# Optimization experiments

Hardware: AMD Instinct MI355X
Metric: run time of the kernel (lower is better)

## Reference

```python
import jax, jax.numpy as jnp
import numpy as np

HEADS = 16
CHUNK = 128  # chunked (mathematically exact) form of the causal cumsum linear attention
EPS = 0.001


def _linear_attention(q, k, v):
    # q, k, v: (B, H, L, d); q, k already SiLU-featurized
    B, H, L, d = q.shape
    Nc = L // CHUNK
    qc = q.reshape(B, H, Nc, CHUNK, d)
    kc = k.reshape(B, H, Nc, CHUNK, d)
    vc = v.reshape(B, H, Nc, CHUNK, d)

    # inter-chunk running state: S = cumsum of k (x) v over previous chunks, z = cumsum of k
    kv_chunk = jnp.einsum('bhncd,bhnce->bhnde', kc, vc)        # (B,H,Nc,d,d)
    S = jnp.cumsum(kv_chunk, axis=2) - kv_chunk                 # exclusive cumsum
    k_sum = kc.sum(axis=3)                                      # (B,H,Nc,d)
    z = jnp.cumsum(k_sum, axis=2) - k_sum                       # exclusive cumsum

    # intra-chunk causal part
    scores = jnp.einsum('bhnid,bhnjd->bhnij', qc, kc)           # (B,H,Nc,C,C)
    mask = jnp.tril(jnp.ones((CHUNK, CHUNK), dtype=bool))
    scores = jnp.where(mask, scores, jnp.zeros((), scores.dtype))
    num = jnp.einsum('bhnij,bhnje->bhnie', scores, vc)
    num = num + jnp.einsum('bhnid,bhnde->bhnie', qc, S)

    k_cum_local = jnp.cumsum(kc, axis=3)                        # within-chunk cumsum of k
    den = jnp.einsum('bhnid,bhnid->bhni', qc, k_cum_local)
    den = den + jnp.einsum('bhnid,bhnd->bhni', qc, z)

    out = num / jnp.maximum(den, EPS)[..., None]
    return out.reshape(B, H, L, d)


def setup_inputs() -> dict:
    key = jax.random.key(0)
    ks = jax.random.split(key, 9)
    D = 1024
    B, L = 4, 2048
    s = 0.02  # init scale
    return {
        'x':  jax.random.normal(ks[0], (B, L, D), dtype=jnp.float32),
        'Wq': jax.random.normal(ks[1], (D, D), dtype=jnp.float32) * s,
        'bq': jnp.zeros((D,), dtype=jnp.float32),
        'Wk': jax.random.normal(ks[2], (D, D), dtype=jnp.float32) * s,
        'bk': jnp.zeros((D,), dtype=jnp.float32),
        'Wv': jax.random.normal(ks[3], (D, D), dtype=jnp.float32) * s,
        'bv': jnp.zeros((D,), dtype=jnp.float32),
        'Wo': jax.random.normal(ks[4], (D, D), dtype=jnp.float32) * s,
        'bo': jnp.zeros((D,), dtype=jnp.float32),
    }


def reference(x, Wq, bq, Wk, bk, Wv, bv, Wo, bo):
    B, L, D = x.shape
    H = HEADS
    d = D // H
    # torch Linear: y = x @ W.T + b
    q = jax.nn.silu(x @ Wq.T + bq).reshape(B, L, H, d).transpose(0, 2, 1, 3)
    k = jax.nn.silu(x @ Wk.T + bk).reshape(B, L, H, d).transpose(0, 2, 1, 3)
    v = (x @ Wv.T + bv).reshape(B, L, H, d).transpose(0, 2, 1, 3)
    out = _linear_attention(q, k, v)                  # (B,H,L,d)
    out = out.transpose(0, 2, 1, 3).reshape(B, L, D)
    return out @ Wo.T + bo
```

## Files before the change

kernel.cpp:

```cpp
#include <hip/hip_runtime.h>
#include <math.h>

#define D_MODEL 1024
#define HEADS   16
#define HDIM    64
#define CHUNK   128
#define B_SZ    4
#define L_SEQ   2048
#define NCHUNK  16
#define NTOK    8192
#define EPS_DEN 1e-3f

typedef _Float16 half8 __attribute__((ext_vector_type(8)));
typedef _Float16 half4 __attribute__((ext_vector_type(4)));
typedef float    f32x4 __attribute__((ext_vector_type(4)));

__device__ __forceinline__ void gld_lds16(const void* g, void* l) {
    __builtin_amdgcn_global_load_lds(
        (const __attribute__((address_space(1))) void*)g,
        (__attribute__((address_space(3))) void*)l, 16, 0, 0);
}

__global__ __launch_bounds__(256) void prep(
    const float* __restrict__ x,  const float* __restrict__ Wq,
    const float* __restrict__ Wk, const float* __restrict__ Wv,
    const float* __restrict__ Wo, const float* __restrict__ bq,
    const float* __restrict__ bk,
    _Float16* __restrict__ x2,  _Float16* __restrict__ w2q,
    _Float16* __restrict__ w2k, _Float16* __restrict__ wv16,
    _Float16* __restrict__ wo16, float* __restrict__ bqk) {
    const int bid = blockIdx.x;
    if (bid < 5120) {
        const float* src; _Float16* dst; int t;
        if (bid < 4096)      { src = x;  dst = x2;  t = bid * 256 + threadIdx.x; }
        else if (bid < 4608) { src = Wq; dst = w2q; t = (bid - 4096) * 256 + threadIdx.x; }
        else                 { src = Wk; dst = w2k; t = (bid - 4608) * 256 + threadIdx.x; }
        int m = t >> 7, kc = (t & 127) << 3;
        const float* s = src + (size_t)m * 1024 + kc;
        f32x4 a = *(const f32x4*)s;
        f32x4 b = *(const f32x4*)(s + 4);
        float xs[8] = {a.x, a.y, a.z, a.w, b.x, b.y, b.z, b.w};
        half8 hi, lo;
        #pragma unroll
        for (int u = 0; u < 8; ++u) {
            _Float16 h = (_Float16)xs[u];
            hi[u] = h;
            lo[u] = (_Float16)(xs[u] - (float)h);
        }
        *(half8*)(dst + (size_t)m * 2048 + kc)        = hi;
        *(half8*)(dst + (size_t)m * 2048 + 1024 + kc) = lo;
    } else if (bid < 6144) {
        const float* src; _Float16* dst; int t;
        if (bid < 5632) { src = Wv; dst = wv16; t = (bid - 5120) * 256 + threadIdx.x; }
        else            { src = Wo; dst = wo16; t = (bid - 5632) * 256 + threadIdx.x; }
        int m = t >> 7, kc = (t & 127) << 3;
        const float* s = src + (size_t)m * 1024 + kc;
        f32x4 a = *(const f32x4*)s;
        f32x4 b = *(const f32x4*)(s + 4);
        float xs[8] = {a.x, a.y, a.z, a.w, b.x, b.y, b.z, b.w};
        half8 hv;
        #pragma unroll
        for (int u = 0; u < 8; ++u) hv[u] = (_Float16)xs[u];
        *(half8*)(dst + (size_t)m * 1024 + kc) = hv;
    } else {
        int i = (bid - 6144) * 256 + threadIdx.x;
        bqk[i] = (i < 1024) ? bq[i] : bk[i - 1024];
    }
}

__global__ __launch_bounds__(256, 4) void gemm_qkv(
    const _Float16* __restrict__ A,
    const _Float16* __restrict__ Bqk,
    const _Float16* __restrict__ Bv,
    const float* __restrict__ bqk, const float* __restrict__ bv,
    _Float16* __restrict__ Qlo, _Float16* __restrict__ Klo,
    _Float16* __restrict__ Q16, _Float16* __restrict__ K16,
    _Float16* __restrict__ V16, float* __restrict__ ksum) {
    __shared__ __align__(16) _Float16 sbuf[2 * 8192];
    __shared__ float sksum[2][128];
    _Float16* sC16 = sbuf;

    const int cb   = blockIdx.y;
    const int isqk = (cb < 16);
    const int isk  = (cb >= 8 && cb < 16);
    const int tid  = threadIdx.x;
    const int lane = tid & 63;
    const int w    = tid >> 6;
    const int row0 = blockIdx.x * 128;
    const int col0 = cb * 128;
    const int wm   = (w & 1) * 64;
    const int wn   = (w >> 1) * 64;

    const _Float16* B = isqk ? Bqk : Bv;
    const int ldb     = isqk ? 2048 : 1024;
    const int bcol0   = isqk ? col0 : col0 - 2048;
    const int kits    = isqk ? 64 : 32;

    const int ch0 = w * 64 + lane;
    const int rS0 = ch0 >> 2;
    const int cS0 = (ch0 & 3) ^ ((rS0 >> 1) & 3);
    const int ch1 = ch0 + 256;
    const int rS1 = ch1 >> 2;
    const int cS1 = (ch1 & 3) ^ ((rS1 >> 1) & 3);

    const _Float16* gA0 = A + (size_t)(row0  + rS0) * 2048 + cS0 * 8;
    const _Float16* gA1 = A + (size_t)(row0  + rS1) * 2048 + cS1 * 8;
    const _Float16* gB0 = B + (size_t)(bcol0 + rS0) * ldb  + cS0 * 8;
    const _Float16* gB1 = B + (size_t)(bcol0 + rS1) * ldb  + cS1 * 8;

    auto stage = [&](int kt, int bsel) {
        const int k0   = kt * 32;
        const int acol = k0;
        const int bcol = (k0 < 1024) ? k0 : k0 - 1024;
        _Float16* l = sbuf + bsel * 8192;
        gld_lds16(gA0 + acol, l + w * 512);
        gld_lds16(gA1 + acol, l + 2048 + w * 512);
        gld_lds16(gB0 + bcol, l + 4096 + w * 512);
        gld_lds16(gB1 + bcol, l + 6144 + w * 512);
    };

    f32x4 acc[4][4];
    #pragma unroll
    for (int i = 0; i < 4; ++i)
        #pragma unroll
        for (int j = 0; j < 4; ++j) { f32x4 z = {0.f, 0.f, 0.f, 0.f}; acc[i][j] = z; }

    const int ml = lane & 15;
    const int kg = lane >> 4;
    int offA[4], offB[4];
    #pragma unroll
    for (int i = 0; i < 4; ++i) {
        int r  = wm + i * 16 + ml;
        offA[i] = r * 32 + (kg ^ ((r >> 1) & 3)) * 8;
        int rn = wn + i * 16 + ml;
        offB[i] = 4096 + rn * 32 + (kg ^ ((rn >> 1) & 3)) * 8;
    }

    stage(0, 0);
    asm volatile("s_waitcnt vmcnt(0)\n\ts_barrier" ::: "memory");
    int cur = 0;
    for (int t = 0; t < kits; ++t) {
        if (t + 1 < kits) stage(t + 1, cur ^ 1);
        const _Float16* lb = sbuf + cur * 8192;
        half8 af[4], bf[4];
        #pragma unroll
        for (int i = 0; i < 4; ++i) {
            af[i] = *(const half8*)&lb[offA[i]];
            bf[i] = *(const half8*)&lb[offB[i]];
        }
        __builtin_amdgcn_s_setprio(1);
        #pragma unroll
        for (int i = 0; i < 4; ++i)
            #pragma unroll
            for (int j = 0; j < 4; ++j)
                acc[i][j] = __builtin_amdgcn_mfma_f32_16x16x32_f16(af[i], bf[j], acc[i][j], 0, 0, 0);
        __builtin_amdgcn_s_setprio(0);
        asm volatile("s_waitcnt vmcnt(0)\n\ts_barrier" ::: "memory");
        cur ^= 1;
    }

    const int colq = isqk ? ((col0 < 1024) ? col0 : col0 - 1024) : (col0 - 2048);
    _Float16* Ylo  = (col0 < 1024) ? Qlo : Klo;
    _Float16* Y16  = isqk ? ((col0 < 1024) ? Q16 : K16) : V16;

    const int rg = lane >> 4;
    #pragma unroll
    for (int j = 0; j < 4; ++j) {
        const float bvb = isqk ? bqk[col0 + wn + j * 16 + ml]
                               : bv[colq + wn + j * 16 + ml];
        const int nn = colq + wn + j * 16 + ml;
        #pragma unroll
        for (int i = 0; i < 4; ++i) {
            #pragma unroll
            for (int t = 0; t < 4; ++t) {
                float vv = acc[i][j][t] + bvb;
                if (isqk) {
                    vv = vv / (1.f + expf(-vv));
                    int mm = row0 + wm + i * 16 + rg * 4 + t;
                    _Float16 hv = (_Float16)vv;
                    Ylo[(size_t)mm * 1024 + nn] = (_Float16)(vv - (float)hv);
                }
                acc[i][j][t] = vv;
            }
        }
    }

    if (isk) {
        #pragma unroll
        for (int j = 0; j < 4; ++j) {
            float ps = 0.f;
            #pragma unroll
            for (int i = 0; i < 4; ++i)
                #pragma unroll
                for (int t = 0; t < 4; ++t) ps += acc[i][j][t];
            ps += __shfl_xor(ps, 16, 64);
            ps += __shfl_xor(ps, 32, 64);
            if (kg == 0) sksum[wm >> 6][wn + j * 16 + ml] = ps;
        }
        __syncthreads();
        if (tid < 128) {
            const int b = row0 >> 11;
            const int n = (row0 >> 7) & 15;
            const int cg = colq + tid;
            const int h = cg >> 6, f = cg & 63;
            ksum[(size_t)(((b * 16 + h) * 16 + n)) * 64 + f] =
                sksum[0][tid] + sksum[1][tid];
        }
        __syncthreads();
    }

    for (int s = 0; s < 4; ++s) {
        if ((wm == 0) == (s < 2)) {
            const int ib = (s & 1) * 2;
            #pragma unroll
            for (int ii = 0; ii < 2; ++ii)
                #pragma unroll
                for (int j = 0; j < 4; ++j)
                    #pragma unroll
                    for (int t = 0; t < 4; ++t) {
                        int lr = ii * 16 + rg * 4 + t;
                        sC16[lr * 136 + wn + j * 16 + ml] = (_Float16)acc[ib + ii][j][t];
                    }
        }
        __syncthreads();
        #pragma unroll
        for (int u = 0; u < 2; ++u) {
            int c = u * 256 + tid;
            int r = c >> 4, cc = (c & 15) * 8;
            half8 hv = *(const half8*)&sC16[r * 136 + cc];
            *(half8*)(Y16 + (size_t)(row0 + 32 * s + r) * 1024 + colq + cc) = hv;
        }
        __syncthreads();
    }
}

__global__ __launch_bounds__(256, 4) void gemm_out(
    const _Float16* __restrict__ A,
    const _Float16* __restrict__ B,
    const float* __restrict__ bias,
    float* __restrict__ Y) {
    __shared__ __align__(16) _Float16 sbuf[2 * 8192];

    const int tid  = threadIdx.x;
    const int lane = tid & 63;
    const int w    = tid >> 6;
    const int row0 = blockIdx.x * 128;
    const int col0 = blockIdx.y * 128;
    const int wm   = (w & 1) * 64;
    const int wn   = (w >> 1) * 64;

    const int ch0 = w * 64 + lane;
    const int rS0 = ch0 >> 2;
    const int cS0 = (ch0 & 3) ^ ((rS0 >> 1) & 3);
    const int ch1 = ch0 + 256;
    const int rS1 = ch1 >> 2;
    const int cS1 = (ch1 & 3) ^ ((rS1 >> 1) & 3);

    const _Float16* gA0 = A + (size_t)(row0 + rS0) * 1024 + cS0 * 8;
    const _Float16* gA1 = A + (size_t)(row0 + rS1) * 1024 + cS1 * 8;
    const _Float16* gB0 = B + (size_t)(col0 + rS0) * 1024 + cS0 * 8;
    const _Float16* gB1 = B + (size_t)(col0 + rS1) * 1024 + cS1 * 8;

    auto stage = [&](int kt, int bsel) {
        const int k0 = kt * 32;
        _Float16* l = sbuf + bsel * 8192;
        gld_lds16(gA0 + k0, l + w * 512);
        gld_lds16(gA1 + k0, l + 2048 + w * 512);
        gld_lds16(gB0 + k0, l + 4096 + w * 512);
        gld_lds16(gB1 + k0, l + 6144 + w * 512);
    };

    f32x4 acc[4][4];
    #pragma unroll
    for (int i = 0; i < 4; ++i)
        #pragma unroll
        for (int j = 0; j < 4; ++j) { f32x4 z = {0.f, 0.f, 0.f, 0.f}; acc[i][j] = z; }

    const int ml = lane & 15;
    const int kg = lane >> 4;
    int offA[4], offB[4];
    #pragma unroll
    for (int i = 0; i < 4; ++i) {
        int r  = wm + i * 16 + ml;
        offA[i] = r * 32 + (kg ^ ((r >> 1) & 3)) * 8;
        int rn = wn + i * 16 + ml;
        offB[i] = 4096 + rn * 32 + (kg ^ ((rn >> 1) & 3)) * 8;
    }

    stage(0, 0);
    asm volatile("s_waitcnt vmcnt(0)\n\ts_barrier" ::: "memory");
    int cur = 0;
    for (int kit = 0; kit < 32; ++kit) {
        if (kit + 1 < 32) stage(kit + 1, cur ^ 1);
        const _Float16* lb = sbuf + cur * 8192;
        half8 af[4], bf[4];
        #pragma unroll
        for (int i = 0; i < 4; ++i) {
            af[i] = *(const half8*)&lb[offA[i]];
            bf[i] = *(const half8*)&lb[offB[i]];
        }
        __builtin_amdgcn_s_setprio(1);
        #pragma unroll
        for (int i = 0; i < 4; ++i)
            #pragma unroll
            for (int j = 0; j < 4; ++j)
                acc[i][j] = __builtin_amdgcn_mfma_f32_16x16x32_f16(af[i], bf[j], acc[i][j], 0, 0, 0);
        __builtin_amdgcn_s_setprio(0);
        asm volatile("s_waitcnt vmcnt(0)\n\ts_barrier" ::: "memory");
        cur ^= 1;
    }

    const int rg = lane >> 4;
    #pragma unroll
    for (int j = 0; j < 4; ++j) {
        const int nn = col0 + wn + j * 16 + ml;
        const float bvb = bias[nn];
        #pragma unroll
        for (int i = 0; i < 4; ++i) {
            #pragma unroll
            for (int t = 0; t < 4; ++t) {
                int mm = row0 + wm + i * 16 + rg * 4 + t;
                Y[(size_t)mm * 1024 + nn] = acc[i][j][t] * 64.f + bvb;
            }
        }
    }
}

__global__ __launch_bounds__(256) void chunk_stats(
    const _Float16* __restrict__ k16g, const _Float16* __restrict__ v16g,
    float* __restrict__ kvT) {
    const int blk = blockIdx.x;
    const int n = blk & 15, bh = blk >> 4, h = bh & 15, b = bh >> 4;
    const size_t base = ((size_t)b * L_SEQ + (size_t)n * CHUNK) * D_MODEL + (size_t)h * HDIM;

    __shared__ __align__(16) _Float16 sv[64 * 136];
    __shared__ __align__(16) _Float16 sk[64 * 136];

    const int tid = threadIdx.x;
    #pragma unroll
    for (int p = 0; p < 4; ++p) {
        int idx = p * 256 + tid;
        int j = idx >> 3, c = idx & 7;
        half8 vv = *(const half8*)(v16g + base + (size_t)j * D_MODEL + c * 8);
        half8 kk = *(const half8*)(k16g + base + (size_t)j * D_MODEL + c * 8);
        #pragma unroll
        for (int u = 0; u < 8; ++u) {
            sv[(c * 8 + u) * 136 + j] = vv[u];
            sk[(c * 8 + u) * 136 + j] = kk[u];
        }
    }
    __syncthreads();

    const int lane = tid & 63;
    const int w    = tid >> 6;
    const int ml   = lane & 15;
    const int kg   = lane >> 4;

    f32x4 acc[4];
    #pragma unroll
    for (int ft = 0; ft < 4; ++ft) { f32x4 z = {0.f,0.f,0.f,0.f}; acc[ft] = z; }
    #pragma unroll
    for (int ft = 0; ft < 4; ++ft)
        #pragma unroll
        for (int kit = 0; kit < 4; ++kit) {
            half8 af = *(const half8*)&sv[(w * 16 + ml) * 136 + kit * 32 + kg * 8];
            half8 bf = *(const half8*)&sk[(ft * 16 + ml) * 136 + kit * 32 + kg * 8];
            acc[ft] = __builtin_amdgcn_mfma_f32_16x16x32_f16(af, bf, acc[ft], 0, 0, 0);
        }
    float* o = kvT + (size_t)blk * 4096;
    #pragma unroll
    for (int ft = 0; ft < 4; ++ft)
        #pragma unroll
        for (int t = 0; t < 4; ++t) {
            int e = w * 16 + kg * 4 + t;
            o[e * 64 + ft * 16 + ml] = acc[ft][t];
        }
}

__global__ __launch_bounds__(256) void scan_chunks(const float* __restrict__ kvT,
                                                   _Float16* __restrict__ kv16,
                                                   float* __restrict__ ksum) {
    const int bh  = blockIdx.x >> 4;
    const int seg = blockIdx.x & 15;
    const int idx = seg * 256 + threadIdx.x;
    const float* base = kvT + (size_t)bh * NCHUNK * 4096 + idx;
    _Float16*   obase = kv16 + (size_t)bh * NCHUNK * 4096 + idx;
    float run = 0.f;
    #pragma unroll
    for (int nn = 0; nn < NCHUNK; ++nn) {
        float t = base[(size_t)nn * 4096];
        obase[(size_t)nn * 4096] = (_Float16)run;
        run += t;
    }
    if (seg == 0 && threadIdx.x < 64) {
        float* zb = ksum + (size_t)bh * NCHUNK * 64 + threadIdx.x;
        float r2 = 0.f;
        #pragma unroll
        for (int nn = 0; nn < NCHUNK; ++nn) {
            float t = zb[nn * 64];
            zb[nn * 64] = r2;
            r2 += t;
        }
    }
}

__global__ __launch_bounds__(256) void attn_core(
    const _Float16* __restrict__ q16g, const _Float16* __restrict__ k16g,
    const _Float16* __restrict__ v16g, const _Float16* __restrict__ qlog,
    const _Float16* __restrict__ klog, const _Float16* __restrict__ ST16,
    const float* __restrict__ zg, _Float16* __restrict__ O16) {
    const int blk = blockIdx.x;
    const int n = blk & 15, bh = blk >> 4, h = bh & 15, b = bh >> 4;
    const size_t base = ((size_t)b * L_SEQ + (size_t)n * CHUNK) * D_MODEL + (size_t)h * HDIM;

    __shared__ __align__(16) _Float16 sq [128 * 72];
    __shared__ __align__(16) _Float16 sk [128 * 72];
    __shared__ __align__(16) _Float16 sv [64 * 136];
    __shared__ __align__(16) _Float16 sS [64 * 72];
    __shared__ __align__(16) _Float16 ssc[64 * 136];
    __shared__ float szz[64];
    _Float16* sklo = ssc;

    const int tid = threadIdx.x;
    #pragma unroll
    for (int p = 0; p < 4; ++p) {
        int idx = p * 256 + tid;
        int j = idx >> 3, c = idx & 7;
        *(half8*)&sq[j * 72 + c * 8] = *(const half8*)(q16g + base + (size_t)j * D_MODEL + c * 8);
        *(half8*)&sk[j * 72 + c * 8] = *(const half8*)(k16g + base + (size_t)j * D_MODEL + c * 8);
        half8 vv = *(const half8*)(v16g + base + (size_t)j * D_MODEL + c * 8);
        #pragma unroll
        for (int u = 0; u < 8; ++u) sv[(c * 8 + u) * 136 + j] = vv[u];
        half8 kl = *(const half8*)(klog + base + (size_t)j * D_MODEL + c * 8);
        *(half8*)&sklo[j * 64 + ((c ^ (j & 7)) << 3)] = kl;
    }
    #pragma unroll
    for (int p = 0; p < 2; ++p) {
        int idx = p * 256 + tid;
        int e = idx >> 3, c = idx & 7;
        *(half8*)&sS[e * 72 + c * 8] =
            *(const half8*)(ST16 + (size_t)blk * 4096 + e * 64 + c * 8);
    }
    if (tid < 64) szz[tid] = zg[(size_t)blk * 64 + tid];
    __syncthreads();

    const int lane = tid & 63;
    const int w    = tid >> 6;
    const int ml   = lane & 15;
    const int kg   = lane >> 4;

    f32x4 acc1a[8], acc1b[8];
    #pragma unroll
    for (int nt = 0; nt < 8; ++nt) {
        f32x4 z = {0.f,0.f,0.f,0.f}; acc1a[nt] = z; acc1b[nt] = z;
    }

    auto qk_acc = [&](f32x4 (&a1)[8], int r0) {
        const int rowmax = r0 + 15;
        half8 aflo0 = *(const half8*)(qlog + base + (size_t)(r0 + ml) * D_MODEL + kg * 8);
        half8 aflo1 = *(const half8*)(qlog + base + (size_t)(r0 + ml) * D_MODEL + 32 + kg * 8);
        #pragma unroll
        for (int nt = 0; nt < 8; ++nt) {
            if (nt * 16 <= rowmax) {
                #pragma unroll
                for (int kit = 0; kit < 2; ++kit) {
                    half8 af = *(const half8*)&sq[(r0 + ml) * 72 + kit * 32 + kg * 8];
                    half8 bf = *(const half8*)&sk[(nt * 16 + ml) * 72 + kit * 32 + kg * 8];
                    a1[nt] = __builtin_amdgcn_mfma_f32_16x16x32_f16(af, bf, a1[nt], 0, 0, 0);
                }
            }
        }
        #pragma unroll
        for (int nt = 0; nt < 8; ++nt) {
            if (nt * 16 <= rowmax) {
                const int jr = nt * 16 + ml;
                half8 bl0 = *(const half8*)&sklo[jr * 64 + ((kg ^ (jr & 7)) << 3)];
                half8 bl1 = *(const half8*)&sklo[jr * 64 + (((4 + kg) ^ (jr & 7)) << 3)];
                half8 ah0 = *(const half8*)&sq[(r0 + ml) * 72 + kg * 8];
                half8 ah1 = *(const half8*)&sq[(r0 + ml) * 72 + 32 + kg * 8];
                half8 bh0 = *(const half8*)&sk[jr * 72 + kg * 8];
                half8 bh1 = *(const half8*)&sk[jr * 72 + 32 + kg * 8];
                a1[nt] = __builtin_amdgcn_mfma_f32_16x16x32_f16(ah0, bl0, a1[nt], 0, 0, 0);
                a1[nt] = __builtin_amdgcn_mfma_f32_16x16x32_f16(ah1, bl1, a1[nt], 0, 0, 0);
                a1[nt] = __builtin_amdgcn_mfma_f32_16x16x32_f16(aflo0, bh0, a1[nt], 0, 0, 0);
                a1[nt] = __builtin_amdgcn_mfma_f32_16x16x32_f16(aflo1, bh1, a1[nt], 0, 0, 0);
            }
        }
    };
    qk_acc(acc1a, w * 16);
    qk_acc(acc1b, 64 + w * 16);
    __syncthreads();

    auto finish = [&](f32x4 (&a1)[8], int h2, int nkit) {
        const int r0 = h2 * 64 + w * 16;
        float rs[4];
        #pragma unroll
        for (int t = 0; t < 4; ++t) {
            const int ig = r0 + kg * 4 + t;
            float s = 0.f;
            #pragma unroll
            for (int nt = 0; nt < 8; ++nt) {
                int jg = nt * 16 + ml;
                s += (jg <= ig) ? a1[nt][t] : 0.f;
            }
            const int f0 = ml * 4;
            half4 ql = *(const half4*)(qlog + base + (size_t)ig * D_MODEL + f0);
            #pragma unroll
            for (int u = 0; u < 4; ++u)
                s += ((float)sq[ig * 72 + f0 + u] + (float)ql[u]) * szz[f0 + u];
            s += __shfl_xor(s, 1, 64);
            s += __shfl_xor(s, 2, 64);
            s += __shfl_xor(s, 4, 64);
            s += __shfl_xor(s, 8, 64);
            rs[t] = s;
        }

        #pragma unroll
        for (int nt = 0; nt < 8; ++nt) {
            #pragma unroll
            for (int t = 0; t < 4; ++t) {
                int lr = w * 16 + kg * 4 + t;
                int ig = h2 * 64 + lr;
                int jg = nt * 16 + ml;
                float val = (jg <= ig) ? a1[nt][t] : 0.f;
                ssc[lr * 136 + jg] = (_Float16)val;
            }
        }
        __syncthreads();

        f32x4 acc2[4];
        #pragma unroll
        for (int et = 0; et < 4; ++et) { f32x4 z = {0.f,0.f,0.f,0.f}; acc2[et] = z; }
        #pragma unroll
        for (int et = 0; et < 4; ++et) {
            for (int kit = 0; kit < nkit; ++kit) {
                half8 af = *(const half8*)&ssc[(w * 16 + ml) * 136 + kit * 32 + kg * 8];
                half8 bf = *(const half8*)&sv[(et * 16 + ml) * 136 + kit * 32 + kg * 8];
                acc2[et] = __builtin_amdgcn_mfma_f32_16x16x32_f16(af, bf, acc2[et], 0, 0, 0);
            }
            #pragma unroll
            for (int kit = 0; kit < 2; ++kit) {
                half8 af = *(const half8*)&sq[(r0 + ml) * 72 + kit * 32 + kg * 8];
                half8 bf = *(const half8*)&sS[(et * 16 + ml) * 72 + kit * 32 + kg * 8];
                acc2[et] = __builtin_amdgcn_mfma_f32_16x16x32_f16(af, bf, acc2[et], 0, 0, 0);
            }
        }
        #pragma unroll
        for (int t = 0; t < 4; ++t) {
            int lr = w * 16 + kg * 4 + t;
            int ig = h2 * 64 + lr;
            float rc = 0.015625f / fmaxf(rs[t], EPS_DEN);
            #pragma unroll
            for (int et = 0; et < 4; ++et) {
                int e = et * 16 + ml;
                O16[base + (size_t)ig * D_MODEL + e] = (_Float16)(acc2[et][t] * rc);
            }
        }
        __syncthreads();
    };
    finish(acc1a, 0, 2);
    finish(acc1b, 1, 4);
}

extern "C" void kernel_launch(void* const* d_in, const int* in_sizes, int n_in,
                              void* d_out, int out_size, void* d_ws, size_t ws_size,
                              hipStream_t stream) {
    const float* x  = (const float*)d_in[0];
    const float* Wq = (const float*)d_in[1];
    const float* bq = (const float*)d_in[2];
    const float* Wk = (const float*)d_in[3];
    const float* bk = (const float*)d_in[4];
    const float* Wv = (const float*)d_in[5];
    const float* bv = (const float*)d_in[6];
    const float* Wo = (const float*)d_in[7];
    const float* bo = (const float*)d_in[8];
    float* out = (float*)d_out;

    char* p = (char*)d_ws;
    _Float16* x2   = (_Float16*)p;  p += (size_t)NTOK * 2048 * 2;
    _Float16* w2q  = (_Float16*)p;  p += (size_t)1024 * 2048 * 2;
    _Float16* w2k  = (_Float16*)p;  p += (size_t)1024 * 2048 * 2;
    _Float16* wv16 = (_Float16*)p;  p += (size_t)1024 * 1024 * 2;
    _Float16* wo16 = (_Float16*)p;  p += (size_t)1024 * 1024 * 2;
    _Float16* qlo  = (_Float16*)p;  p += (size_t)NTOK * 1024 * 2;
    _Float16* klo  = (_Float16*)p;  p += (size_t)NTOK * 1024 * 2;
    _Float16* q16  = (_Float16*)p;  p += (size_t)NTOK * 1024 * 2;
    _Float16* k16  = (_Float16*)p;  p += (size_t)NTOK * 1024 * 2;
    _Float16* v16  = (_Float16*)p;  p += (size_t)NTOK * 1024 * 2;
    float* kvT  = (float*)p;        p += (size_t)1024 * 4096 * 4;
    _Float16* kv16 = (_Float16*)p;  p += (size_t)1024 * 4096 * 2;
    float* ksb  = (float*)p;        p += (size_t)1024 * 64 * 4;
    float* bqk  = (float*)p;        p += 2048 * 4;
    _Float16* attn16 = x2;

    prep<<<6152, 256, 0, stream>>>(x, Wq, Wk, Wv, Wo, bq, bk,
                                   x2, w2q, w2k, wv16, wo16, bqk);

    gemm_qkv<<<dim3(64, 24), 256, 0, stream>>>(x2, w2q, wv16, bqk, bv,
                                               qlo, klo, q16, k16, v16, ksb);

    chunk_stats<<<1024, 256, 0, stream>>>(k16, v16, kvT);
    scan_chunks<<<1024, 256, 0, stream>>>(kvT, kv16, ksb);
    attn_core<<<1024, 256, 0, stream>>>(q16, k16, v16, qlo, klo, kv16, ksb, attn16);

    gemm_out<<<dim3(64, 8), 256, 0, stream>>>(attn16, wo16, bo, out);
}
```

Before: 295.5 us.

## Use 512 threads in attn_core so each wave owns one 16-row tile

The attention core block grows from 4 to 8 waves. Each wave now handles one 16-row slice of the 128-row chunk instead of two sequential halves, and the score buffer in shared memory doubles so all 128 rows are staged at once. This removes the serialized two-pass finish and its extra barriers, and halves per-wave accumulator register use. The cost is more LDS per block (ssc grows to 128x136 halfs), which may lower occupancy, and a causal workload that is imbalanced across waves.

New measurement: 294.0 us. No clear change (-0.5%).

```diff
diff --git a/kernel.cpp b/kernel.cpp
--- a/kernel.cpp
+++ b/kernel.cpp
@@ -404,7 +404,7 @@
     }
 }
 
-__global__ __launch_bounds__(256) void attn_core(
+__global__ __launch_bounds__(512) void attn_core(
     const _Float16* __restrict__ q16g, const _Float16* __restrict__ k16g,
     const _Float16* __restrict__ v16g, const _Float16* __restrict__ qlog,
     const _Float16* __restrict__ klog, const _Float16* __restrict__ ST16,
@@ -417,14 +417,14 @@
     __shared__ __align__(16) _Float16 sk [128 * 72];
     __shared__ __align__(16) _Float16 sv [64 * 136];
     __shared__ __align__(16) _Float16 sS [64 * 72];
-    __shared__ __align__(16) _Float16 ssc[64 * 136];
+    __shared__ __align__(16) _Float16 ssc[128 * 136];
     __shared__ float szz[64];
     _Float16* sklo = ssc;
 
     const int tid = threadIdx.x;
     #pragma unroll
-    for (int p = 0; p < 4; ++p) {
-        int idx = p * 256 + tid;
+    for (int p = 0; p < 2; ++p) {
+        int idx = p * 512 + tid;
         int j = idx >> 3, c = idx & 7;
         *(half8*)&sq[j * 72 + c * 8] = *(const half8*)(q16g + base + (size_t)j * D_MODEL + c * 8);
         *(half8*)&sk[j * 72 + c * 8] = *(const half8*)(k16g + base + (size_t)j * D_MODEL + c * 8);
@@ -434,10 +434,8 @@
         half8 kl = *(const half8*)(klog + base + (size_t)j * D_MODEL + c * 8);
         *(half8*)&sklo[j * 64 + ((c ^ (j & 7)) << 3)] = kl;
     }
-    #pragma unroll
-    for (int p = 0; p < 2; ++p) {
-        int idx = p * 256 + tid;
-        int e = idx >> 3, c = idx & 7;
+    {
+        int e = tid >> 3, c = tid & 7;
         *(half8*)&sS[e * 72 + c * 8] =
             *(const half8*)(ST16 + (size_t)blk * 4096 + e * 64 + c * 8);
     }
@@ -448,118 +446,107 @@
     const int w    = tid >> 6;
     const int ml   = lane & 15;
     const int kg   = lane >> 4;
-
-    f32x4 acc1a[8], acc1b[8];
+    const int r0   = w * 16;
+    const int rowmax = r0 + 15;
+
+    f32x4 acc1[8];
+    #pragma unroll
+    for (int nt = 0; nt < 8; ++nt) { f32x4 z = {0.f,0.f,0.f,0.f}; acc1[nt] = z; }
+
+    half8 aflo0 = *(const half8*)(qlog + base + (size_t)(r0 + ml) * D_MODEL + kg * 8);
+    half8 aflo1 = *(const half8*)(qlog + base + (size_t)(r0 + ml) * D_MODEL + 32 + kg * 8);
     #pragma unroll
     for (int nt = 0; nt < 8; ++nt) {
-        f32x4 z = {0.f,0.f,0.f,0.f}; acc1a[nt] = z; acc1b[nt] = z;
-    }
-
-    auto qk_acc = [&](f32x4 (&a1)[8], int r0) {
-        const int rowmax = r0 + 15;
-        half8 aflo0 = *(const half8*)(qlog + base + (size_t)(r0 + ml) * D_MODEL + kg * 8);
-        half8 aflo1 = *(const half8*)(qlog + base + (size_t)(r0 + ml) * D_MODEL + 32 + kg * 8);
-        #pragma unroll
-        for (int nt = 0; nt < 8; ++nt) {
-            if (nt * 16 <= rowmax) {
-                #pragma unroll
-                for (int kit = 0; kit < 2; ++kit) {
-                    half8 af = *(const half8*)&sq[(r0 + ml) * 72 + kit * 32 + kg * 8];
-                    half8 bf = *(const half8*)&sk[(nt * 16 + ml) * 72 + kit * 32 + kg * 8];
-                    a1[nt] = __builtin_amdgcn_mfma_f32_16x16x32_f16(af, bf, a1[nt], 0, 0, 0);
-                }
-            }
-        }
-        #pragma unroll
-        for (int nt = 0; nt < 8; ++nt) {
-            if (nt * 16 <= rowmax) {
-                const int jr = nt * 16 + ml;
-                half8 bl0 = *(const half8*)&sklo[jr * 64 + ((kg ^ (jr & 7)) << 3)];
-                half8 bl1 = *(const half8*)&sklo[jr * 64 + (((4 + kg) ^ (jr & 7)) << 3)];
-                half8 ah0 = *(const half8*)&sq[(r0 + ml) * 72 + kg * 8];
-                half8 ah1 = *(const half8*)&sq[(r0 + ml) * 72 + 32 + kg * 8];
-                half8 bh0 = *(const half8*)&sk[jr * 72 + kg * 8];
-                half8 bh1 = *(const half8*)&sk[jr * 72 + 32 + kg * 8];
-                a1[nt] = __builtin_amdgcn_mfma_f32_16x16x32_f16(ah0, bl0, a1[nt], 0, 0, 0);
-                a1[nt] = __builtin_amdgcn_mfma_f32_16x16x32_f16(ah1, bl1, a1[nt], 0, 0, 0);
-                a1[nt] = __builtin_amdgcn_mfma_f32_16x16x32_f16(aflo0, bh0, a1[nt], 0, 0, 0);
-                a1[nt] = __builtin_amdgcn_mfma_f32_16x16x32_f16(aflo1, bh1, a1[nt], 0, 0, 0);
-            }
-        }
-    };
-    qk_acc(acc1a, w * 16);
-    qk_acc(acc1b, 64 + w * 16);
-    __syncthreads();
-
-    auto finish = [&](f32x4 (&a1)[8], int h2, int nkit) {
-        const int r0 = h2 * 64 + w * 16;
-        float rs[4];
-        #pragma unroll
-        for (int t = 0; t < 4; ++t) {
-            const int ig = r0 + kg * 4 + t;
-            float s = 0.f;
-            #pragma unroll
-            for (int nt = 0; nt < 8; ++nt) {
-                int jg = nt * 16 + ml;
-                s += (jg <= ig) ? a1[nt][t] : 0.f;
-            }
-            const int f0 = ml * 4;
-            half4 ql = *(const half4*)(qlog + base + (size_t)ig * D_MODEL + f0);
-            #pragma unroll
-            for (int u = 0; u < 4; ++u)
-                s += ((float)sq[ig * 72 + f0 + u] + (float)ql[u]) * szz[f0 + u];
-            s += __shfl_xor(s, 1, 64);
-            s += __shfl_xor(s, 2, 64);
-            s += __shfl_xor(s, 4, 64);
-            s += __shfl_xor(s, 8, 64);
-            rs[t] = s;
-        }
-
-        #pragma unroll
-        for (int nt = 0; nt < 8; ++nt) {
-            #pragma unroll
-            for (int t = 0; t < 4; ++t) {
-                int lr = w * 16 + kg * 4 + t;
-                int ig = h2 * 64 + lr;
-                int jg = nt * 16 + ml;
-                float val = (jg <= ig) ? a1[nt][t] : 0.f;
-                ssc[lr * 136 + jg] = (_Float16)val;
-            }
-        }
-        __syncthreads();
-
-        f32x4 acc2[4];
-        #pragma unroll
-        for (int et = 0; et < 4; ++et) { f32x4 z = {0.f,0.f,0.f,0.f}; acc2[et] = z; }
-        #pragma unroll
-        for (int et = 0; et < 4; ++et) {
-            for (int kit = 0; kit < nkit; ++kit) {
-                half8 af = *(const half8*)&ssc[(w * 16 + ml) * 136 + kit * 32 + kg * 8];
-                half8 bf = *(const half8*)&sv[(et * 16 + ml) * 136 + kit * 32 + kg * 8];
-                acc2[et] = __builtin_amdgcn_mfma_f32_16x16x32_f16(af, bf, acc2[et], 0, 0, 0);
-            }
+        if (nt * 16 <= rowmax) {
             #pragma unroll
             for (int kit = 0; kit < 2; ++kit) {
                 half8 af = *(const half8*)&sq[(r0 + ml) * 72 + kit * 32 + kg * 8];
-                half8 bf = *(const half8*)&sS[(et * 16 + ml) * 72 + kit * 32 + kg * 8];
-                acc2[et] = __builtin_amdgcn_mfma_f32_16x16x32_f16(af, bf, acc2[et], 0, 0, 0);
+                half8 bf = *(const half8*)&sk[(nt * 16 + ml) * 72 + kit * 32 + kg * 8];
+                acc1[nt] = __builtin_amdgcn_mfma_f32_16x16x32_f16(af, bf, acc1[nt], 0, 0, 0);
             }
         }
+    }
+    #pragma unroll
+    for (int nt = 0; nt < 8; ++nt) {
+        if (nt * 16 <= rowmax) {
+            const int jr = nt * 16 + ml;
+            half8 bl0 = *(const half8*)&sklo[jr * 64 + ((kg ^ (jr & 7)) << 3)];
+            half8 bl1 = *(const half8*)&sklo[jr * 64 + (((4 + kg) ^ (jr & 7)) << 3)];
+            half8 ah0 = *(const half8*)&sq[(r0 + ml) * 72 + kg * 8];
+            half8 ah1 = *(const half8*)&sq[(r0 + ml) * 72 + 32 + kg * 8];
+            half8 bh0 = *(const half8*)&sk[jr * 72 + kg * 8];
+            half8 bh1 = *(const half8*)&sk[jr * 72 + 32 + kg * 8];
+            acc1[nt] = __builtin_amdgcn_mfma_f32_16x16x32_f16(ah0, bl0, acc1[nt], 0, 0, 0);
+            acc1[nt] = __builtin_amdgcn_mfma_f32_16x16x32_f16(ah1, bl1, acc1[nt], 0, 0, 0);
+            acc1[nt] = __builtin_amdgcn_mfma_f32_16x16x32_f16(aflo0, bh0, acc1[nt], 0, 0, 0);
+            acc1[nt] = __builtin_amdgcn_mfma_f32_16x16x32_f16(aflo1, bh1, acc1[nt], 0, 0, 0);
+        }
+    }
+
+    float rs[4];
+    #pragma unroll
+    for (int t = 0; t < 4; ++t) {
+        const int ig = r0 + kg * 4 + t;
+        float s = 0.f;
+        #pragma unroll
+        for (int nt = 0; nt < 8; ++nt) {
+            int jg = nt * 16 + ml;
+            s += (jg <= ig) ? acc1[nt][t] : 0.f;
+        }
+        const int f0 = ml * 4;
+        half4 ql = *(const half4*)(qlog + base + (size_t)ig * D_MODEL + f0);
+        #pragma unroll
+        for (int u = 0; u < 4; ++u)
+            s += ((float)sq[ig * 72 + f0 + u] + (float)ql[u]) * szz[f0 + u];
+        s += __shfl_xor(s, 1, 64);
+        s += __shfl_xor(s, 2, 64);
+        s += __shfl_xor(s, 4, 64);
+        s += __shfl_xor(s, 8, 64);
+        rs[t] = s;
+    }
+
+    __syncthreads();
+
+    #pragma unroll
+    for (int nt = 0; nt < 8; ++nt) {
         #pragma unroll
         for (int t = 0; t < 4; ++t) {
-            int lr = w * 16 + kg * 4 + t;
-            int ig = h2 * 64 + lr;
-            float rc = 0.015625f / fmaxf(rs[t], EPS_DEN);
-            #pragma unroll
-            for (int et = 0; et < 4; ++et) {
-                int e = et * 16 + ml;
-                O16[base + (size_t)ig * D_MODEL + e] = (_Float16)(acc2[et][t] * rc);
-            }
-        }
-        __syncthreads();
-    };
-    finish(acc1a, 0, 2);
-    finish(acc1b, 1, 4);
+            int lr = r0 + kg * 4 + t;
+            int jg = nt * 16 + ml;
+            float val = (jg <= lr) ? acc1[nt][t] : 0.f;
+            ssc[lr * 136 + jg] = (_Float16)val;
+        }
+    }
+    __syncthreads();
+
+    const int nkit = (w >> 1) + 1;
+    f32x4 acc2[4];
+    #pragma unroll
+    for (int et = 0; et < 4; ++et) { f32x4 z = {0.f,0.f,0.f,0.f}; acc2[et] = z; }
+    #pragma unroll
+    for (int et = 0; et < 4; ++et) {
+        for (int kit = 0; kit < nkit; ++kit) {
+            half8 af = *(const half8*)&ssc[(r0 + ml) * 136 + kit * 32 + kg * 8];
+            half8 bf = *(const half8*)&sv[(et * 16 + ml) * 136 + kit * 32 + kg * 8];
+            acc2[et] = __builtin_amdgcn_mfma_f32_16x16x32_f16(af, bf, acc2[et], 0, 0, 0);
+        }
+        #pragma unroll
+        for (int kit = 0; kit < 2; ++kit) {
+            half8 af = *(const half8*)&sq[(r0 + ml) * 72 + kit * 32 + kg * 8];
+            half8 bf = *(const half8*)&sS[(et * 16 + ml) * 72 + kit * 32 + kg * 8];
+            acc2[et] = __builtin_amdgcn_mfma_f32_16x16x32_f16(af, bf, acc2[et], 0, 0, 0);
+        }
+    }
+    #pragma unroll
+    for (int t = 0; t < 4; ++t) {
+        int ig = r0 + kg * 4 + t;
+        float rc = 0.015625f / fmaxf(rs[t], EPS_DEN);
+        #pragma unroll
+        for (int et = 0; et < 4; ++et) {
+            int e = et * 16 + ml;
+            O16[base + (size_t)ig * D_MODEL + e] = (_Float16)(acc2[et][t] * rc);
+        }
+    }
 }
 
 extern "C" void kernel_launch(void* const* d_in, const int* in_sizes, int n_in,
@@ -601,7 +588,7 @@
 
     chunk_stats<<<1024, 256, 0, stream>>>(k16, v16, kvT);
     scan_chunks<<<1024, 256, 0, stream>>>(kvT, kv16, ksb);
-    attn_core<<<1024, 256, 0, stream>>>(q16, k16, v16, qlo, klo, kv16, ksb, attn16);
+    attn_core<<<1024, 512, 0, stream>>>(q16, k16, v16, qlo, klo, kv16, ksb, attn16);
 
     gemm_out<<<dim3(64, 8), 256, 0, stream>>>(attn16, wo16, bo, out);
 }
```
